# Performance work log

Measured on AMD Instinct MI355X. Metric: run time of the kernel, lower is better.

Reference implementation:

```python
import jax, jax.numpy as jnp
import numpy as np

B, N, D, F, H, C, L = 64, 8192, 5, 16, 4, 4, 4
NEG_SLOPE = 0.2


def setup_inputs() -> dict:
    key = jax.random.key(0)
    ks = jax.random.split(key, 16)
    lin = lambda k, fi, fo: (jax.random.normal(k, (fi, fo), jnp.float32) / np.sqrt(fi)).astype(jnp.float32)
    x = jax.random.normal(ks[0], (B, N, F), jnp.float32)
    agent_nodes = jax.random.randint(ks[1], (B,), 0, N, dtype=jnp.int32)
    neighbors = jax.random.randint(ks[2], (N, D), 0, N, dtype=jnp.int32)
    # GATv2 params (L layers, all 16 -> 4 heads x 4 = 16)
    Wl = jax.random.normal(ks[3], (L, F, H, C), jnp.float32) / np.sqrt(F)
    Wr = jax.random.normal(ks[4], (L, F, H, C), jnp.float32) / np.sqrt(F)
    att_w = jax.random.normal(ks[5], (L, H, C), jnp.float32) / np.sqrt(C)
    bias = jnp.zeros((L, H * C), jnp.float32)
    # global classifier 16->32->64, edge classifier 99->16->8->1
    Wg1, bg1 = lin(ks[6], H * C, 2 * H * C), jnp.zeros(2 * H * C, jnp.float32)
    Wg2, bg2 = lin(ks[7], 2 * H * C, 4 * H * C), jnp.zeros(4 * H * C, jnp.float32)
    e_in = 2 * H * C + 3 + 4 * H * C  # 99
    We1, be1 = lin(ks[8], e_in, H * C), jnp.zeros(H * C, jnp.float32)
    We2, be2 = lin(ks[9], H * C, H * C // 2), jnp.zeros(H * C // 2, jnp.float32)
    We3, be3 = lin(ks[10], H * C // 2, 1), jnp.zeros(1, jnp.float32)
    return dict(x=x, agent_nodes=agent_nodes, neighbors=neighbors, Wl=Wl, Wr=Wr,
                att_w=att_w, bias=bias, Wg1=Wg1, bg1=bg1, Wg2=Wg2, bg2=bg2,
                We1=We1, be1=be1, We2=We2, be2=be2, We3=We3, be3=be3)


def _gatv2_layer(h, src, dst, wl, wr, a, b, n_nodes):
    # h: [B,N,Fin]; wl/wr: [Fin,H,C]; a: [H,C]; b: [H*C]
    xl = jnp.einsum('bnf,fhc->bnhc', h, wl)   # source transform
    xr = jnp.einsum('bnf,fhc->bnhc', h, wr)   # target transform
    hs = xl[:, src]                            # [B,E,H,C]
    ht = xr[:, dst]
    logit = jnp.einsum('behc,hc->beh', jax.nn.leaky_relu(hs + ht, NEG_SLOPE), a)
    lt = logit.transpose(1, 0, 2)              # [E,B,H] (segment ops need E first)
    m = jax.ops.segment_max(lt, dst, num_segments=n_nodes)
    w = jnp.exp(lt - m[dst])
    s = jax.ops.segment_sum(w, dst, num_segments=n_nodes)
    alpha = w / (s[dst] + 1e-16)               # [E,B,H] softmax over in-edges of dst
    msg = alpha[..., None] * hs.transpose(1, 0, 2, 3)
    out = jax.ops.segment_sum(msg, dst, num_segments=n_nodes)  # [N,B,H,C]
    return out.transpose(1, 0, 2, 3).reshape(h.shape[0], n_nodes, -1) + b


def reference(x, agent_nodes, neighbors, Wl, Wr, att_w, bias,
              Wg1, bg1, Wg2, bg2, We1, be1, We2, be2, We3, be3):
    Bn, Nn, _ = x.shape
    Dd = neighbors.shape[1]
    loop = jnp.arange(Nn, dtype=neighbors.dtype)
    src = jnp.concatenate([jnp.repeat(loop, Dd), loop])   # add_self_loops
    dst = jnp.concatenate([neighbors.reshape(-1), loop])
    h = x
    for i in range(Wl.shape[0]):
        h = _gatv2_layer(h, src, dst, Wl[i], Wr[i], att_w[i], bias[i], Nn)
    # global mean aggregation -> 2 SlimFC(tanh)
    agg = jnp.tanh(h.mean(axis=1) @ Wg1 + bg1)
    agg = jnp.tanh(agg @ Wg2 + bg2)                        # [B,64]
    # agent out-edges: source node + its D neighbors
    nb = neighbors[agent_nodes]                            # [B,D]
    bi = jnp.arange(Bn)
    source = h[bi, agent_nodes]                            # [B,16]
    target = h[bi[:, None], nb]                            # [B,D,16]
    tok = jnp.eye(3, dtype=h.dtype)                        # 3 one-hot act tokens
    feats = jnp.concatenate([
        jnp.broadcast_to(source[:, None, None, :], (Bn, 3, Dd, source.shape[-1])),
        jnp.broadcast_to(tok[None, :, None, :], (Bn, 3, Dd, 3)),
        jnp.broadcast_to(target[:, None, :, :], (Bn, 3, Dd, target.shape[-1])),
        jnp.broadcast_to(agg[:, None, None, :], (Bn, 3, Dd, agg.shape[-1])),
    ], axis=-1)                                            # [B,3,D,99]
    e = jnp.tanh(feats @ We1 + be1)
    e = jnp.tanh(e @ We2 + be2)
    e = (e @ We3 + be3)[..., 0]                            # [B,3,D]
    # logits[b, turn*D + move] (convert_multidiscrete_action_to_discrete)
    return e.reshape(Bn, 3 * Dd)
```

## Files before the change

### kernel.cpp

```cpp
#include <hip/hip_runtime.h>
#include <hip/hip_fp16.h>
#include <cmath>

#define NNODES 8192
#define NB 64
#define ND 5
#define MAXDEG 64
#define NBLK_T0 2048
#define NBLK_LAY 8192



__global__ void __launch_bounds__(256)
k_t0fill(const float* __restrict__ x, const float* __restrict__ Wl0, const float* __restrict__ Wr0,
         __half* __restrict__ xl0, __half* __restrict__ xr0,
         const int* __restrict__ agent, const int* __restrict__ nbr,
         int* __restrict__ cnt, int* __restrict__ slot, int* __restrict__ needed) {
  if (blockIdx.x >= NBLK_T0) {
    int eb = blockIdx.x - NBLK_T0;
    if (eb < 160) {
      int i = eb*256 + threadIdx.x;
      int v = nbr[i];
      int pos = atomicAdd(&cnt[v], 1);
      slot[v*MAXDEG + 1 + pos] = i/ND;
    } else if (threadIdx.x < NB) {
      int an = agent[threadIdx.x];
      needed[an] = 1;
      #pragma unroll
      for (int d = 0; d < ND; ++d) needed[nbr[an*ND + d]] = 1;
    }
    return;
  }
  int gid = blockIdx.x*blockDim.x + threadIdx.x;
  int n = gid >> 6;
  int b = gid & 63;
  const float4* src = (const float4*)(x + (((size_t)b*NNODES + n) << 4));
  float hv[16];
  #pragma unroll
  for (int q = 0; q < 4; ++q) *(float4*)(hv+4*q) = src[q];
  float yl[16], yr[16];
  #pragma unroll
  for (int j = 0; j < 16; ++j) { yl[j] = 0.f; yr[j] = 0.f; }
  #pragma unroll
  for (int f = 0; f < 16; ++f) {
    float hf = hv[f];
    #pragma unroll
    for (int j = 0; j < 16; ++j) {
      yl[j] = fmaf(hf, Wl0[f*16+j], yl[j]);
      yr[j] = fmaf(hf, Wr0[f*16+j], yr[j]);
    }
  }
  size_t idx = ((size_t)n << 10) + (b << 4);
  __half2 lh[8], rh[8];
  #pragma unroll
  for (int j = 0; j < 8; ++j) {
    lh[j] = __floats2half2_rn(yl[2*j], yl[2*j+1]);
    rh[j] = __floats2half2_rn(yr[2*j], yr[2*j+1]);
  }
  float4* ld = (float4*)(xl0 + idx);
  ld[0] = *(float4*)&lh[0]; ld[1] = *(float4*)&lh[4];
  float4* rd = (float4*)(xr0 + idx);
  rd[0] = *(float4*)&rh[0]; rd[1] = *(float4*)&rh[4];
}


template<bool LAST>
__global__ void __launch_bounds__(256)
k_layer(const __half* __restrict__ xlin, const __half* __restrict__ xrin,
        __half* __restrict__ xlout, __half* __restrict__ xrout,
        const float* __restrict__ WlNext, const float* __restrict__ WrNext,
        const float* __restrict__ att, const float* __restrict__ bias,
        const int* __restrict__ cnt, const int* __restrict__ slot,
        const int* __restrict__ needed, __half* __restrict__ h,
        float* __restrict__ meanpart) {
  __shared__ float sW[544];
  __shared__ float msm[4][16][17];
  int tid = threadIdx.x;
  int w = tid >> 6, lane = tid & 63;

  if (!LAST) {
    sW[tid]     = WlNext[tid];
    sW[256+tid] = WrNext[tid];
  }
  if (tid < 16)      sW[512+tid]    = att[tid];
  else if (tid < 32) sW[512+tid]    = bias[tid-16];
  __syncthreads();

  int wv = (blockIdx.x << 2) + w;
  int q = wv >> 13;
  int v = wv & (NNODES-1);
  int head = lane & 3;
  size_t soff = ((size_t)q << 8) + (lane << 2);

  float4 awv = *(float4*)&sW[512 + head*4];
  float aw0 = awv.x, aw1 = awv.y, aw2 = awv.z, aw3 = awv.w;

  float xr0, xr1, xr2, xr3;
  {
    float2 rx = *(const float2*)(xrin + (((size_t)v) << 10) + soff);
    __half2* ph = (__half2*)&rx;
    float2 f0 = __half22float2(ph[0]), f1 = __half22float2(ph[1]);
    xr0 = f0.x; xr1 = f0.y; xr2 = f1.x; xr3 = f1.y;
  }

  float s = 0.f, a0 = 0.f, a1 = 0.f, a2 = 0.f, a3 = 0.f;
  int deg = cnt[v];
  int tot = deg + 1;
  const int* sl = slot + v*MAXDEG;

  auto loadrow = [&](int u) -> float2 {
    return *(const float2*)(xlin + (((size_t)u) << 10) + soff);
  };
  auto process = [&](float2 r) {
    __half2* ph = (__half2*)&r;
    float2 f0 = __half22float2(ph[0]), f1 = __half22float2(ph[1]);
    float t0 = f0.x, t1 = f0.y, t2 = f1.x, t3 = f1.y;
    float z0 = t0 + xr0; z0 = (z0 >= 0.f) ? z0 : 0.2f*z0;
    float z1 = t1 + xr1; z1 = (z1 >= 0.f) ? z1 : 0.2f*z1;
    float z2 = t2 + xr2; z2 = (z2 >= 0.f) ? z2 : 0.2f*z2;
    float z3 = t3 + xr3; z3 = (z3 >= 0.f) ? z3 : 0.2f*z3;
    float lg = fmaf(z0, aw0, fmaf(z1, aw1, fmaf(z2, aw2, z3*aw3)));
    float p = __expf(lg);
    s += p;
    a0 = fmaf(p, t0, a0); a1 = fmaf(p, t1, a1);
    a2 = fmaf(p, t2, a2); a3 = fmaf(p, t3, a3);
  };

  float2 r0, r1, r2, r3, r4, r5, r6, r7, pA, pB;
  r0 = loadrow(v);
  if (tot > 1) r1 = loadrow(sl[1]);
  if (tot > 2) r2 = loadrow(sl[2]);
  if (tot > 3) r3 = loadrow(sl[3]);
  if (tot > 4) r4 = loadrow(sl[4]);
  if (tot > 5) r5 = loadrow(sl[5]);
  if (tot > 6) r6 = loadrow(sl[6]);
  if (tot > 7) r7 = loadrow(sl[7]);
  if (tot > 8) pA = loadrow(sl[8]);
  if (tot > 9) pB = loadrow(sl[9]);
  process(r0);
  if (tot > 1) process(r1);
  if (tot > 2) process(r2);
  if (tot > 3) process(r3);
  if (tot > 4) process(r4);
  if (tot > 5) process(r5);
  if (tot > 6) process(r6);
  if (tot > 7) process(r7);
  int e = 8;
  for (; e+1 < tot; e += 2) {
    float2 cA = pA; if (e+2 < tot) pA = loadrow(sl[e+2]);
    float2 cB = pB; if (e+3 < tot) pB = loadrow(sl[e+3]);
    process(cA); process(cB);
  }
  if (e < tot) process(pA);

  float inv = 1.f / s;
  float4 bsv = *(float4*)&sW[528 + head*4];
  float o0 = fmaf(a0, inv, bsv.x), o1 = fmaf(a1, inv, bsv.y);
  float o2 = fmaf(a2, inv, bsv.z), o3 = fmaf(a3, inv, bsv.w);

  if (!LAST) {
    float of[16];
    int lb = lane & ~3;
    #pragma unroll
    for (int src = 0; src < 4; ++src) {
      of[src*4+0] = __shfl(o0, lb+src);
      of[src*4+1] = __shfl(o1, lb+src);
      of[src*4+2] = __shfl(o2, lb+src);
      of[src*4+3] = __shfl(o3, lb+src);
    }
    float yl0=0.f, yl1=0.f, yl2=0.f, yl3=0.f;
    float yr0=0.f, yr1=0.f, yr2=0.f, yr3=0.f;
    #pragma unroll
    for (int f = 0; f < 16; ++f) {
      float4 wl4 = *(float4*)&sW[f*16 + head*4];
      float4 wr4 = *(float4*)&sW[256 + f*16 + head*4];
      float ofv = of[f];
      yl0 = fmaf(ofv, wl4.x, yl0); yl1 = fmaf(ofv, wl4.y, yl1);
      yl2 = fmaf(ofv, wl4.z, yl2); yl3 = fmaf(ofv, wl4.w, yl3);
      yr0 = fmaf(ofv, wr4.x, yr0); yr1 = fmaf(ofv, wr4.y, yr1);
      yr2 = fmaf(ofv, wr4.z, yr2); yr3 = fmaf(ofv, wr4.w, yr3);
    }
    float2 lo, ro;
    ((__half2*)&lo)[0] = __floats2half2_rn(yl0, yl1);
    ((__half2*)&lo)[1] = __floats2half2_rn(yl2, yl3);
    ((__half2*)&ro)[0] = __floats2half2_rn(yr0, yr1);
    ((__half2*)&ro)[1] = __floats2half2_rn(yr2, yr3);
    size_t idx = (((size_t)v) << 10) + soff;
    *(float2*)(xlout + idx) = lo;
    *(float2*)(xrout + idx) = ro;
  } else {
    if (needed[v]) {
      float2 ho;
      ((__half2*)&ho)[0] = __floats2half2_rn(o0, o1);
      ((__half2*)&ho)[1] = __floats2half2_rn(o2, o3);
      *(float2*)(h + (((size_t)v) << 10) + soff) = ho;
    }
    int bl = lane >> 2;
    msm[w][bl][head*4+0] = o0;
    msm[w][bl][head*4+1] = o1;
    msm[w][bl][head*4+2] = o2;
    msm[w][bl][head*4+3] = o3;
    __syncthreads();
    int bl2 = tid >> 4, hc = tid & 15;
    float ssum = msm[0][bl2][hc] + msm[1][bl2][hc] + msm[2][bl2][hc] + msm[3][bl2][hc];
    meanpart[(size_t)blockIdx.x*256 + tid] = ssum;
  }
}


__global__ void __launch_bounds__(256)
k_tail(const __half* __restrict__ h, const int* __restrict__ agent,
       const int* __restrict__ nbr, const float* __restrict__ meanpart,
       const float* __restrict__ Wg1, const float* __restrict__ bg1,
       const float* __restrict__ Wg2, const float* __restrict__ bg2,
       const float* __restrict__ We1, const float* __restrict__ be1,
       const float* __restrict__ We2, const float* __restrict__ be2,
       const float* __restrict__ We3, const float* __restrict__ be3,
       float* __restrict__ out) {
  int b = blockIdx.x;
  int t = threadIdx.x;
  __shared__ float red[256];
  __shared__ float mean[16], g1[32], aggs[64];
  __shared__ float srcv[16];
  __shared__ float tgt[5][16];
  __shared__ float e1s[15][16];
  __shared__ float e2s[15][8];
  int an = agent[b];

  {
    int hc = t & 15, grp = t >> 4;
    int q = b >> 4, bl = b & 15;
    float s = 0.f;
    int base = q*2048 + grp*128;
    #pragma unroll 8
    for (int p = 0; p < 128; ++p)
      s += meanpart[(size_t)(base+p)*256 + bl*16 + hc];
    red[t] = s;
    __syncthreads();
    if (t < 16) {
      float m = 0.f;
      for (int g = 0; g < 16; ++g) m += red[g*16 + t];
      mean[t] = m * (1.0f/NNODES);
    }
  }
  if (t >= 64 && t < 80) srcv[t-64] = __half2float(h[((size_t)an << 10) + (b << 4) + (t-64)]);
  if (t >= 96 && t < 176) {
    int d = (t-96)/16, k = (t-96)%16;
    int nn = nbr[an*ND + d];
    tgt[d][k] = __half2float(h[((size_t)nn << 10) + (b << 4) + k]);
  }
  __syncthreads();
  if (t < 32) {
    float a = bg1[t];
    for (int f = 0; f < 16; ++f) a = fmaf(mean[f], Wg1[f*32+t], a);
    g1[t] = tanhf(a);
  }
  __syncthreads();
  if (t < 64) {
    float a = bg2[t];
    for (int f = 0; f < 32; ++f) a = fmaf(g1[f], Wg2[f*64+t], a);
    aggs[t] = tanhf(a);
  }
  __syncthreads();
  if (t < 240) {
    int j = t & 15, td = t >> 4;
    int tk = td/5, d = td%5;
    float a = be1[j];
    for (int k = 0; k < 16; ++k) a = fmaf(srcv[k],  We1[k*16+j],      a);
    a += We1[(16+tk)*16 + j];
    for (int k = 0; k < 16; ++k) a = fmaf(tgt[d][k], We1[(19+k)*16+j], a);
    for (int k = 0; k < 64; ++k) a = fmaf(aggs[k],  We1[(35+k)*16+j], a);
    e1s[td][j] = tanhf(a);
  }
  __syncthreads();
  if (t < 120) {
    int j = t & 7, td = t >> 3;
    float a = be2[j];
    for (int k = 0; k < 16; ++k) a = fmaf(e1s[td][k], We2[k*8+j], a);
    e2s[td][j] = tanhf(a);
  }
  __syncthreads();
  if (t < 15) {
    float a = be3[0];
    for (int k = 0; k < 8; ++k) a = fmaf(e2s[t][k], We3[k], a);
    out[b*15 + t] = a;
  }
}


extern "C" void kernel_launch(void* const* d_in, const int* in_sizes, int n_in,
                              void* d_out, int out_size, void* d_ws, size_t ws_size,
                              hipStream_t stream) {
  const float* x     = (const float*)d_in[0];
  const int*   agent = (const int*)  d_in[1];
  const int*   nbr   = (const int*)  d_in[2];
  const float* Wl    = (const float*)d_in[3];
  const float* Wr    = (const float*)d_in[4];
  const float* att   = (const float*)d_in[5];
  const float* bias  = (const float*)d_in[6];
  const float* Wg1   = (const float*)d_in[7];
  const float* bg1   = (const float*)d_in[8];
  const float* Wg2   = (const float*)d_in[9];
  const float* bg2   = (const float*)d_in[10];
  const float* We1   = (const float*)d_in[11];
  const float* be1   = (const float*)d_in[12];
  const float* We2   = (const float*)d_in[13];
  const float* be2   = (const float*)d_in[14];
  const float* We3   = (const float*)d_in[15];
  const float* be3   = (const float*)d_in[16];
  float* out = (float*)d_out;

  char* ws = (char*)d_ws;
  size_t off = 0;
  auto alloc = [&](size_t bytes) -> void* {
    void* p = ws + off;
    off += (bytes + 255) & ~(size_t)255;
    return p;
  };
  const size_t XBYTES = (size_t)NNODES*NB*16*sizeof(__half);
  __half* h    = (__half*)alloc(XBYTES);
  __half* xlA  = (__half*)alloc(XBYTES);
  __half* xlB  = (__half*)alloc(XBYTES);
  __half* xrA  = (__half*)alloc(XBYTES);
  __half* xrB  = (__half*)alloc(XBYTES);
  int*  slot   = (int*)alloc((size_t)NNODES*MAXDEG*sizeof(int));
  float* meanpart = (float*)alloc((size_t)NBLK_LAY*256*sizeof(float));
  int* cnt    = (int*)alloc(NNODES*sizeof(int));
  int* needed = (int*)alloc(NNODES*sizeof(int));

  hipMemsetAsync(cnt, 0, NNODES*sizeof(int)*2, stream);

  k_t0fill<<<NBLK_T0 + 161, 256, 0, stream>>>(x, Wl, Wr, xlA, xrA,
                                              agent, nbr, cnt, slot, needed);

  k_layer<false><<<NBLK_LAY, 256, 0, stream>>>(xlA, xrA, xlB, xrB, Wl + 256, Wr + 256,
                                               att,      bias,      cnt, slot, needed, nullptr, nullptr);
  k_layer<false><<<NBLK_LAY, 256, 0, stream>>>(xlB, xrB, xlA, xrA, Wl + 512, Wr + 512,
                                               att + 16, bias + 16, cnt, slot, needed, nullptr, nullptr);
  k_layer<false><<<NBLK_LAY, 256, 0, stream>>>(xlA, xrA, xlB, xrB, Wl + 768, Wr + 768,
                                               att + 32, bias + 32, cnt, slot, needed, nullptr, nullptr);
  k_layer<true ><<<NBLK_LAY, 256, 0, stream>>>(xlB, xrB, nullptr, nullptr, nullptr, nullptr,
                                               att + 48, bias + 48, cnt, slot, needed, h, meanpart);

  k_tail<<<NB, 256, 0, stream>>>(h, agent, nbr, meanpart,
                                 Wg1, bg1, Wg2, bg2,
                                 We1, be1, We2, be2, We3, be3, out);
}
```

Before: 244.3 us.

## Split per-node GAT work so each lane handles two channels instead of four

The layer kernel now gives each lane two feature channels (8 lanes per batch element, 8 batch elements per wavefront) instead of four channels for 16 batch elements, and doubles the number of blocks. The attention logit is completed with a cross-lane xor shuffle between the two lanes of a head. The goal is more wavefronts in flight to hide the latency of the irregular neighbor gathers, at the cost of narrower 4-byte loads, an extra shuffle per edge, and neighbor-list and index loads repeated across twice as many wavefronts. The mean-partial buffer and the tail reduction indexing are adjusted to match.

```diff
diff --git a/kernel.cpp b/kernel.cpp
--- a/kernel.cpp
+++ b/kernel.cpp
@@ -7,7 +7,7 @@
 #define ND 5
 #define MAXDEG 64
 #define NBLK_T0 2048
-#define NBLK_LAY 8192
+#define NBLK_LAY 16384
 
 
 
@@ -74,7 +74,7 @@
         const int* __restrict__ needed, __half* __restrict__ h,
         float* __restrict__ meanpart) {
   __shared__ float sW[544];
-  __shared__ float msm[4][16][17];
+  __shared__ float msm[4][8][17];
   int tid = threadIdx.x;
   int w = tid >> 6, lane = tid & 63;
 
@@ -87,46 +87,43 @@
   __syncthreads();
 
   int wv = (blockIdx.x << 2) + w;
-  int q = wv >> 13;
+  int e = wv >> 13;
   int v = wv & (NNODES-1);
-  int head = lane & 3;
-  size_t soff = ((size_t)q << 8) + (lane << 2);
-
-  float4 awv = *(float4*)&sW[512 + head*4];
-  float aw0 = awv.x, aw1 = awv.y, aw2 = awv.z, aw3 = awv.w;
-
-  float xr0, xr1, xr2, xr3;
+  int bb = lane >> 3;
+  int k  = lane & 7;
+  size_t soff = ((size_t)e << 7) + (bb << 4) + (k << 1);
+
+  float2 awv = *(float2*)&sW[512 + 2*k];
+  float aw0 = awv.x, aw1 = awv.y;
+
+  float xr0, xr1;
   {
-    float2 rx = *(const float2*)(xrin + (((size_t)v) << 10) + soff);
-    __half2* ph = (__half2*)&rx;
-    float2 f0 = __half22float2(ph[0]), f1 = __half22float2(ph[1]);
-    xr0 = f0.x; xr1 = f0.y; xr2 = f1.x; xr3 = f1.y;
-  }
-
-  float s = 0.f, a0 = 0.f, a1 = 0.f, a2 = 0.f, a3 = 0.f;
+    float rx = *(const float*)(xrin + (((size_t)v) << 10) + soff);
+    float2 f0 = __half22float2(*(__half2*)&rx);
+    xr0 = f0.x; xr1 = f0.y;
+  }
+
+  float s = 0.f, a0 = 0.f, a1 = 0.f;
   int deg = cnt[v];
   int tot = deg + 1;
   const int* sl = slot + v*MAXDEG;
 
-  auto loadrow = [&](int u) -> float2 {
-    return *(const float2*)(xlin + (((size_t)u) << 10) + soff);
+  auto loadrow = [&](int u) -> float {
+    return *(const float*)(xlin + (((size_t)u) << 10) + soff);
   };
-  auto process = [&](float2 r) {
-    __half2* ph = (__half2*)&r;
-    float2 f0 = __half22float2(ph[0]), f1 = __half22float2(ph[1]);
-    float t0 = f0.x, t1 = f0.y, t2 = f1.x, t3 = f1.y;
+  auto process = [&](float r) {
+    float2 f0 = __half22float2(*(__half2*)&r);
+    float t0 = f0.x, t1 = f0.y;
     float z0 = t0 + xr0; z0 = (z0 >= 0.f) ? z0 : 0.2f*z0;
     float z1 = t1 + xr1; z1 = (z1 >= 0.f) ? z1 : 0.2f*z1;
-    float z2 = t2 + xr2; z2 = (z2 >= 0.f) ? z2 : 0.2f*z2;
-    float z3 = t3 + xr3; z3 = (z3 >= 0.f) ? z3 : 0.2f*z3;
-    float lg = fmaf(z0, aw0, fmaf(z1, aw1, fmaf(z2, aw2, z3*aw3)));
+    float lgh = fmaf(z0, aw0, z1*aw1);
+    float lg = lgh + __shfl_xor(lgh, 1);
     float p = __expf(lg);
     s += p;
     a0 = fmaf(p, t0, a0); a1 = fmaf(p, t1, a1);
-    a2 = fmaf(p, t2, a2); a3 = fmaf(p, t3, a3);
   };
 
-  float2 r0, r1, r2, r3, r4, r5, r6, r7, pA, pB;
+  float r0, r1, r2, r3, r4, r5, r6, r7, pA, pB;
   r0 = loadrow(v);
   if (tot > 1) r1 = loadrow(sl[1]);
   if (tot > 2) r2 = loadrow(sl[2]);
@@ -145,65 +142,50 @@
   if (tot > 5) process(r5);
   if (tot > 6) process(r6);
   if (tot > 7) process(r7);
-  int e = 8;
-  for (; e+1 < tot; e += 2) {
-    float2 cA = pA; if (e+2 < tot) pA = loadrow(sl[e+2]);
-    float2 cB = pB; if (e+3 < tot) pB = loadrow(sl[e+3]);
+  int ei = 8;
+  for (; ei+1 < tot; ei += 2) {
+    float cA = pA; if (ei+2 < tot) pA = loadrow(sl[ei+2]);
+    float cB = pB; if (ei+3 < tot) pB = loadrow(sl[ei+3]);
     process(cA); process(cB);
   }
-  if (e < tot) process(pA);
+  if (ei < tot) process(pA);
 
   float inv = 1.f / s;
-  float4 bsv = *(float4*)&sW[528 + head*4];
+  float2 bsv = *(float2*)&sW[528 + 2*k];
   float o0 = fmaf(a0, inv, bsv.x), o1 = fmaf(a1, inv, bsv.y);
-  float o2 = fmaf(a2, inv, bsv.z), o3 = fmaf(a3, inv, bsv.w);
 
   if (!LAST) {
     float of[16];
-    int lb = lane & ~3;
+    int lb = lane & ~7;
     #pragma unroll
-    for (int src = 0; src < 4; ++src) {
-      of[src*4+0] = __shfl(o0, lb+src);
-      of[src*4+1] = __shfl(o1, lb+src);
-      of[src*4+2] = __shfl(o2, lb+src);
-      of[src*4+3] = __shfl(o3, lb+src);
-    }
-    float yl0=0.f, yl1=0.f, yl2=0.f, yl3=0.f;
-    float yr0=0.f, yr1=0.f, yr2=0.f, yr3=0.f;
+    for (int m = 0; m < 8; ++m) {
+      of[2*m]   = __shfl(o0, lb+m);
+      of[2*m+1] = __shfl(o1, lb+m);
+    }
+    float yl0=0.f, yl1=0.f, yr0=0.f, yr1=0.f;
     #pragma unroll
     for (int f = 0; f < 16; ++f) {
-      float4 wl4 = *(float4*)&sW[f*16 + head*4];
-      float4 wr4 = *(float4*)&sW[256 + f*16 + head*4];
+      float2 wl2 = *(float2*)&sW[f*16 + 2*k];
+      float2 wr2 = *(float2*)&sW[256 + f*16 + 2*k];
       float ofv = of[f];
-      yl0 = fmaf(ofv, wl4.x, yl0); yl1 = fmaf(ofv, wl4.y, yl1);
-      yl2 = fmaf(ofv, wl4.z, yl2); yl3 = fmaf(ofv, wl4.w, yl3);
-      yr0 = fmaf(ofv, wr4.x, yr0); yr1 = fmaf(ofv, wr4.y, yr1);
-      yr2 = fmaf(ofv, wr4.z, yr2); yr3 = fmaf(ofv, wr4.w, yr3);
-    }
-    float2 lo, ro;
-    ((__half2*)&lo)[0] = __floats2half2_rn(yl0, yl1);
-    ((__half2*)&lo)[1] = __floats2half2_rn(yl2, yl3);
-    ((__half2*)&ro)[0] = __floats2half2_rn(yr0, yr1);
-    ((__half2*)&ro)[1] = __floats2half2_rn(yr2, yr3);
+      yl0 = fmaf(ofv, wl2.x, yl0); yl1 = fmaf(ofv, wl2.y, yl1);
+      yr0 = fmaf(ofv, wr2.x, yr0); yr1 = fmaf(ofv, wr2.y, yr1);
+    }
     size_t idx = (((size_t)v) << 10) + soff;
-    *(float2*)(xlout + idx) = lo;
-    *(float2*)(xrout + idx) = ro;
+    *(__half2*)(xlout + idx) = __floats2half2_rn(yl0, yl1);
+    *(__half2*)(xrout + idx) = __floats2half2_rn(yr0, yr1);
   } else {
     if (needed[v]) {
-      float2 ho;
-      ((__half2*)&ho)[0] = __floats2half2_rn(o0, o1);
-      ((__half2*)&ho)[1] = __floats2half2_rn(o2, o3);
-      *(float2*)(h + (((size_t)v) << 10) + soff) = ho;
-    }
-    int bl = lane >> 2;
-    msm[w][bl][head*4+0] = o0;
-    msm[w][bl][head*4+1] = o1;
-    msm[w][bl][head*4+2] = o2;
-    msm[w][bl][head*4+3] = o3;
+      *(__half2*)(h + (((size_t)v) << 10) + soff) = __floats2half2_rn(o0, o1);
+    }
+    msm[w][bb][2*k]   = o0;
+    msm[w][bb][2*k+1] = o1;
     __syncthreads();
-    int bl2 = tid >> 4, hc = tid & 15;
-    float ssum = msm[0][bl2][hc] + msm[1][bl2][hc] + msm[2][bl2][hc] + msm[3][bl2][hc];
-    meanpart[(size_t)blockIdx.x*256 + tid] = ssum;
+    if (tid < 128) {
+      int bl = tid >> 4, hc = tid & 15;
+      float ssum = msm[0][bl][hc] + msm[1][bl][hc] + msm[2][bl][hc] + msm[3][bl][hc];
+      meanpart[(size_t)blockIdx.x*128 + tid] = ssum;
+    }
   }
 }
 
@@ -229,12 +211,12 @@
 
   {
     int hc = t & 15, grp = t >> 4;
-    int q = b >> 4, bl = b & 15;
+    int e = b >> 3, bl = b & 7;
     float s = 0.f;
-    int base = q*2048 + grp*128;
+    int base = e*2048 + grp*128;
     #pragma unroll 8
     for (int p = 0; p < 128; ++p)
-      s += meanpart[(size_t)(base+p)*256 + bl*16 + hc];
+      s += meanpart[(size_t)(base+p)*128 + bl*16 + hc];
     red[t] = s;
     __syncthreads();
     if (t < 16) {
@@ -324,7 +306,7 @@
   __half* xrA  = (__half*)alloc(XBYTES);
   __half* xrB  = (__half*)alloc(XBYTES);
   int*  slot   = (int*)alloc((size_t)NNODES*MAXDEG*sizeof(int));
-  float* meanpart = (float*)alloc((size_t)NBLK_LAY*256*sizeof(float));
+  float* meanpart = (float*)alloc((size_t)NBLK_LAY*128*sizeof(float));
   int* cnt    = (int*)alloc(NNODES*sizeof(int));
   int* needed = (int*)alloc(NNODES*sizeof(int));
 
```

New measurement: 309.1 us. +26.5%, slower.

## Stage input transform through LDS and fuse tail into last GAT layer

Applied to the files above, without the earlier changes.

The layer-0 transform kernel now loads 8 nodes × 64 batches of x into shared memory with coalesced float4 reads, then computes two batch outputs per thread. This replaces strided per-thread reads of x. The separate tail kernel is removed: the last layer launches 64 extra blocks that spin on a global completion counter, then run the classifier. The fusion saves one launch but depends on the extra blocks not starving the layer blocks, and it adds atomic polling overhead.

```diff
diff --git a/kernel.cpp b/kernel.cpp
--- a/kernel.cpp
+++ b/kernel.cpp
@@ -6,7 +6,7 @@
 #define NB 64
 #define ND 5
 #define MAXDEG 64
-#define NBLK_T0 2048
+#define NBLK_T0 1024
 #define NBLK_LAY 8192
 
 
@@ -31,36 +31,66 @@
     }
     return;
   }
-  int gid = blockIdx.x*blockDim.x + threadIdx.x;
-  int n = gid >> 6;
-  int b = gid & 63;
-  const float4* src = (const float4*)(x + (((size_t)b*NNODES + n) << 4));
-  float hv[16];
+  __shared__ float4 sx4[8*321 + 8];
+  int t = threadIdx.x;
+  int n0 = blockIdx.x * 8;
+
+  {
+    int ln = (t & 31) >> 2;
+    int q  = t & 3;
+    float4 v[8];
+    #pragma unroll
+    for (int it = 0; it < 8; ++it) {
+      int b = it*8 + (t >> 5);
+      v[it] = *(const float4*)(x + ((size_t)b*NNODES + n0 + ln)*16 + q*4);
+    }
+    #pragma unroll
+    for (int it = 0; it < 8; ++it) {
+      int b = it*8 + (t >> 5);
+      sx4[ln*321 + b*5 + q] = v[it];
+    }
+  }
+  __syncthreads();
+
+  int cn = t >> 5;
+  int bq = t & 31;
+  float4 outL[2][2], outR[2][2];
   #pragma unroll
-  for (int q = 0; q < 4; ++q) *(float4*)(hv+4*q) = src[q];
-  float yl[16], yr[16];
+  for (int j = 0; j < 2; ++j) {
+    int b = bq + 32*j;
+    float hv[16];
+    #pragma unroll
+    for (int q = 0; q < 4; ++q) *(float4*)(hv + 4*q) = sx4[cn*321 + b*5 + q];
+    float yl[16], yr[16];
+    #pragma unroll
+    for (int jj = 0; jj < 16; ++jj) { yl[jj] = 0.f; yr[jj] = 0.f; }
+    #pragma unroll
+    for (int f = 0; f < 16; ++f) {
+      float hf = hv[f];
+      #pragma unroll
+      for (int jj = 0; jj < 16; ++jj) {
+        yl[jj] = fmaf(hf, Wl0[f*16+jj], yl[jj]);
+        yr[jj] = fmaf(hf, Wr0[f*16+jj], yr[jj]);
+      }
+    }
+    __half2 lh[8], rh[8];
+    #pragma unroll
+    for (int jj = 0; jj < 8; ++jj) {
+      lh[jj] = __floats2half2_rn(yl[2*jj], yl[2*jj+1]);
+      rh[jj] = __floats2half2_rn(yr[2*jj], yr[2*jj+1]);
+    }
+    outL[j][0] = *(float4*)&lh[0]; outL[j][1] = *(float4*)&lh[4];
+    outR[j][0] = *(float4*)&rh[0]; outR[j][1] = *(float4*)&rh[4];
+  }
   #pragma unroll
-  for (int j = 0; j < 16; ++j) { yl[j] = 0.f; yr[j] = 0.f; }
-  #pragma unroll
-  for (int f = 0; f < 16; ++f) {
-    float hf = hv[f];
-    #pragma unroll
-    for (int j = 0; j < 16; ++j) {
-      yl[j] = fmaf(hf, Wl0[f*16+j], yl[j]);
-      yr[j] = fmaf(hf, Wr0[f*16+j], yr[j]);
-    }
-  }
-  size_t idx = ((size_t)n << 10) + (b << 4);
-  __half2 lh[8], rh[8];
-  #pragma unroll
-  for (int j = 0; j < 8; ++j) {
-    lh[j] = __floats2half2_rn(yl[2*j], yl[2*j+1]);
-    rh[j] = __floats2half2_rn(yr[2*j], yr[2*j+1]);
-  }
-  float4* ld = (float4*)(xl0 + idx);
-  ld[0] = *(float4*)&lh[0]; ld[1] = *(float4*)&lh[4];
-  float4* rd = (float4*)(xr0 + idx);
-  rd[0] = *(float4*)&rh[0]; rd[1] = *(float4*)&rh[4];
+  for (int j = 0; j < 2; ++j) {
+    int b = bq + 32*j;
+    size_t idx = (((size_t)(n0 + cn)) << 10) + (b << 4);
+    float4* ld = (float4*)(xl0 + idx);
+    ld[0] = outL[j][0]; ld[1] = outL[j][1];
+    float4* rd = (float4*)(xr0 + idx);
+    rd[0] = outR[j][0]; rd[1] = outR[j][1];
+  }
 }
 
 
@@ -72,10 +102,95 @@
         const float* __restrict__ att, const float* __restrict__ bias,
         const int* __restrict__ cnt, const int* __restrict__ slot,
         const int* __restrict__ needed, __half* __restrict__ h,
-        float* __restrict__ meanpart) {
+        float* __restrict__ meanpart,
+        const int* __restrict__ agent, const int* __restrict__ nbr,
+        const float* __restrict__ Wg1, const float* __restrict__ bg1,
+        const float* __restrict__ Wg2, const float* __restrict__ bg2,
+        const float* __restrict__ We1, const float* __restrict__ be1,
+        const float* __restrict__ We2, const float* __restrict__ be2,
+        const float* __restrict__ We3, const float* __restrict__ be3,
+        float* __restrict__ out, int* __restrict__ ctr) {
+  int tid = threadIdx.x;
+
+  if (LAST && blockIdx.x >= NBLK_LAY) {
+    int b = blockIdx.x - NBLK_LAY;
+    if (tid == 0) {
+      while (atomicAdd(ctr, 0) < NBLK_LAY) __builtin_amdgcn_s_sleep(16);
+    }
+    __syncthreads();
+    __threadfence();
+
+    __shared__ float red[256];
+    __shared__ float mean[16], g1[32], aggs[64];
+    __shared__ float srcv[16];
+    __shared__ float tgt[5][16];
+    __shared__ float e1s[15][16];
+    __shared__ float e2s[15][8];
+    int an = agent[b];
+
+    {
+      int hc = tid & 15, grp = tid >> 4;
+      int q = b >> 4, bl = b & 15;
+      float s = 0.f;
+      int base = q*2048 + grp*128;
+      #pragma unroll 8
+      for (int p = 0; p < 128; ++p)
+        s += meanpart[(size_t)(base+p)*256 + bl*16 + hc];
+      red[tid] = s;
+      __syncthreads();
+      if (tid < 16) {
+        float m = 0.f;
+        for (int g = 0; g < 16; ++g) m += red[g*16 + tid];
+        mean[tid] = m * (1.0f/NNODES);
+      }
+    }
+    if (tid >= 64 && tid < 80) srcv[tid-64] = __half2float(h[((size_t)an << 10) + (b << 4) + (tid-64)]);
+    if (tid >= 96 && tid < 176) {
+      int d = (tid-96)/16, k = (tid-96)%16;
+      int nn = nbr[an*ND + d];
+      tgt[d][k] = __half2float(h[((size_t)nn << 10) + (b << 4) + k]);
+    }
+    __syncthreads();
+    if (tid < 32) {
+      float a = bg1[tid];
+      for (int f = 0; f < 16; ++f) a = fmaf(mean[f], Wg1[f*32+tid], a);
+      g1[tid] = tanhf(a);
+    }
+    __syncthreads();
+    if (tid < 64) {
+      float a = bg2[tid];
+      for (int f = 0; f < 32; ++f) a = fmaf(g1[f], Wg2[f*64+tid], a);
+      aggs[tid] = tanhf(a);
+    }
+    __syncthreads();
+    if (tid < 240) {
+      int j = tid & 15, td = tid >> 4;
+      int tk = td/5, d = td%5;
+      float a = be1[j];
+      for (int k = 0; k < 16; ++k) a = fmaf(srcv[k],  We1[k*16+j],      a);
+      a += We1[(16+tk)*16 + j];
+      for (int k = 0; k < 16; ++k) a = fmaf(tgt[d][k], We1[(19+k)*16+j], a);
+      for (int k = 0; k < 64; ++k) a = fmaf(aggs[k],  We1[(35+k)*16+j], a);
+      e1s[td][j] = tanhf(a);
+    }
+    __syncthreads();
+    if (tid < 120) {
+      int j = tid & 7, td = tid >> 3;
+      float a = be2[j];
+      for (int k = 0; k < 16; ++k) a = fmaf(e1s[td][k], We2[k*8+j], a);
+      e2s[td][j] = tanhf(a);
+    }
+    __syncthreads();
+    if (tid < 15) {
+      float a = be3[0];
+      for (int k = 0; k < 8; ++k) a = fmaf(e2s[tid][k], We3[k], a);
+      out[b*15 + tid] = a;
+    }
+    return;
+  }
+
   __shared__ float sW[544];
   __shared__ float msm[4][16][17];
-  int tid = threadIdx.x;
   int w = tid >> 6, lane = tid & 63;
 
   if (!LAST) {
@@ -204,86 +319,8 @@
     int bl2 = tid >> 4, hc = tid & 15;
     float ssum = msm[0][bl2][hc] + msm[1][bl2][hc] + msm[2][bl2][hc] + msm[3][bl2][hc];
     meanpart[(size_t)blockIdx.x*256 + tid] = ssum;
-  }
-}
-
-
-__global__ void __launch_bounds__(256)
-k_tail(const __half* __restrict__ h, const int* __restrict__ agent,
-       const int* __restrict__ nbr, const float* __restrict__ meanpart,
-       const float* __restrict__ Wg1, const float* __restrict__ bg1,
-       const float* __restrict__ Wg2, const float* __restrict__ bg2,
-       const float* __restrict__ We1, const float* __restrict__ be1,
-       const float* __restrict__ We2, const float* __restrict__ be2,
-       const float* __restrict__ We3, const float* __restrict__ be3,
-       float* __restrict__ out) {
-  int b = blockIdx.x;
-  int t = threadIdx.x;
-  __shared__ float red[256];
-  __shared__ float mean[16], g1[32], aggs[64];
-  __shared__ float srcv[16];
-  __shared__ float tgt[5][16];
-  __shared__ float e1s[15][16];
-  __shared__ float e2s[15][8];
-  int an = agent[b];
-
-  {
-    int hc = t & 15, grp = t >> 4;
-    int q = b >> 4, bl = b & 15;
-    float s = 0.f;
-    int base = q*2048 + grp*128;
-    #pragma unroll 8
-    for (int p = 0; p < 128; ++p)
-      s += meanpart[(size_t)(base+p)*256 + bl*16 + hc];
-    red[t] = s;
-    __syncthreads();
-    if (t < 16) {
-      float m = 0.f;
-      for (int g = 0; g < 16; ++g) m += red[g*16 + t];
-      mean[t] = m * (1.0f/NNODES);
-    }
-  }
-  if (t >= 64 && t < 80) srcv[t-64] = __half2float(h[((size_t)an << 10) + (b << 4) + (t-64)]);
-  if (t >= 96 && t < 176) {
-    int d = (t-96)/16, k = (t-96)%16;
-    int nn = nbr[an*ND + d];
-    tgt[d][k] = __half2float(h[((size_t)nn << 10) + (b << 4) + k]);
-  }
-  __syncthreads();
-  if (t < 32) {
-    float a = bg1[t];
-    for (int f = 0; f < 16; ++f) a = fmaf(mean[f], Wg1[f*32+t], a);
-    g1[t] = tanhf(a);
-  }
-  __syncthreads();
-  if (t < 64) {
-    float a = bg2[t];
-    for (int f = 0; f < 32; ++f) a = fmaf(g1[f], Wg2[f*64+t], a);
-    aggs[t] = tanhf(a);
-  }
-  __syncthreads();
-  if (t < 240) {
-    int j = t & 15, td = t >> 4;
-    int tk = td/5, d = td%5;
-    float a = be1[j];
-    for (int k = 0; k < 16; ++k) a = fmaf(srcv[k],  We1[k*16+j],      a);
-    a += We1[(16+tk)*16 + j];
-    for (int k = 0; k < 16; ++k) a = fmaf(tgt[d][k], We1[(19+k)*16+j], a);
-    for (int k = 0; k < 64; ++k) a = fmaf(aggs[k],  We1[(35+k)*16+j], a);
-    e1s[td][j] = tanhf(a);
-  }
-  __syncthreads();
-  if (t < 120) {
-    int j = t & 7, td = t >> 3;
-    float a = be2[j];
-    for (int k = 0; k < 16; ++k) a = fmaf(e1s[td][k], We2[k*8+j], a);
-    e2s[td][j] = tanhf(a);
-  }
-  __syncthreads();
-  if (t < 15) {
-    float a = be3[0];
-    for (int k = 0; k < 8; ++k) a = fmaf(e2s[t][k], We3[k], a);
-    out[b*15 + t] = a;
+    __syncthreads();
+    if (tid == 0) { __threadfence(); atomicAdd(ctr, 1); }
   }
 }
 
@@ -327,22 +364,31 @@
   float* meanpart = (float*)alloc((size_t)NBLK_LAY*256*sizeof(float));
   int* cnt    = (int*)alloc(NNODES*sizeof(int));
   int* needed = (int*)alloc(NNODES*sizeof(int));
-
-  hipMemsetAsync(cnt, 0, NNODES*sizeof(int)*2, stream);
+  int* ctr    = (int*)alloc(256);
+
+  hipMemsetAsync(cnt, 0, NNODES*sizeof(int)*2 + 256, stream);
 
   k_t0fill<<<NBLK_T0 + 161, 256, 0, stream>>>(x, Wl, Wr, xlA, xrA,
                                               agent, nbr, cnt, slot, needed);
 
   k_layer<false><<<NBLK_LAY, 256, 0, stream>>>(xlA, xrA, xlB, xrB, Wl + 256, Wr + 256,
-                                               att,      bias,      cnt, slot, needed, nullptr, nullptr);
+                                               att,      bias,      cnt, slot, needed, nullptr, nullptr,
+                                               nullptr, nullptr, nullptr, nullptr, nullptr, nullptr,
+                                               nullptr, nullptr, nullptr, nullptr, nullptr, nullptr,
+                                               nullptr, nullptr);
   k_layer<false><<<NBLK_LAY, 256, 0, stream>>>(xlB, xrB, xlA, xrA, Wl + 512, Wr + 512,
-                                               att + 16, bias + 16, cnt, slot, needed, nullptr, nullptr);
+                                               att + 16, bias + 16, cnt, slot, needed, nullptr, nullptr,
+                                               nullptr, nullptr, nullptr, nullptr, nullptr, nullptr,
+                                               nullptr, nullptr, nullptr, nullptr, nullptr, nullptr,
+                                               nullptr, nullptr);
   k_layer<false><<<NBLK_LAY, 256, 0, stream>>>(xlA, xrA, xlB, xrB, Wl + 768, Wr + 768,
-                                               att + 32, bias + 32, cnt, slot, needed, nullptr, nullptr);
-  k_layer<true ><<<NBLK_LAY, 256, 0, stream>>>(xlB, xrB, nullptr, nullptr, nullptr, nullptr,
-                                               att + 48, bias + 48, cnt, slot, needed, h, meanpart);
-
-  k_tail<<<NB, 256, 0, stream>>>(h, agent, nbr, meanpart,
-                                 Wg1, bg1, Wg2, bg2,
-                                 We1, be1, We2, be2, We3, be3, out);
+                                               att + 32, bias + 32, cnt, slot, needed, nullptr, nullptr,
+                                               nullptr, nullptr, nullptr, nullptr, nullptr, nullptr,
+                                               nullptr, nullptr, nullptr, nullptr, nullptr, nullptr,
+                                               nullptr, nullptr);
+  k_layer<true ><<<NBLK_LAY + NB, 256, 0, stream>>>(xlB, xrB, nullptr, nullptr, nullptr, nullptr,
+                                               att + 48, bias + 48, cnt, slot, needed, h, meanpart,
+                                               agent, nbr, Wg1, bg1, Wg2, bg2,
+                                               We1, be1, We2, be2, We3, be3,
+                                               out, ctr);
 }
```

After: 493.8 us. 102% more time.

## Stage layer-0 input through shared memory for coalesced loads and two batches per thread

Applied to the files above, without the earlier changes.

Each block of the layer-0 transform kernel now handles 8 nodes across all 64 batches. It loads x with coalesced float4 reads, where neighbouring lanes cover consecutive nodes and quarters, and transposes the data through padded shared memory. Each thread then computes two batch rows. Before this, each thread read 64 bytes at a stride of N*16 floats across batches, which left global reads poorly coalesced. The cost is about 41 KB of shared memory per block, which may cap occupancy, and the block count is halved.

```diff
diff --git a/kernel.cpp b/kernel.cpp
--- a/kernel.cpp
+++ b/kernel.cpp
@@ -6,7 +6,7 @@
 #define NB 64
 #define ND 5
 #define MAXDEG 64
-#define NBLK_T0 2048
+#define NBLK_T0 1024
 #define NBLK_LAY 8192
 
 
@@ -31,36 +31,66 @@
     }
     return;
   }
-  int gid = blockIdx.x*blockDim.x + threadIdx.x;
-  int n = gid >> 6;
-  int b = gid & 63;
-  const float4* src = (const float4*)(x + (((size_t)b*NNODES + n) << 4));
-  float hv[16];
+  __shared__ float4 sx4[8*321 + 8];
+  int t = threadIdx.x;
+  int n0 = blockIdx.x * 8;
+
+  {
+    int ln = (t & 31) >> 2;
+    int q  = t & 3;
+    float4 v[8];
+    #pragma unroll
+    for (int it = 0; it < 8; ++it) {
+      int b = it*8 + (t >> 5);
+      v[it] = *(const float4*)(x + ((size_t)b*NNODES + n0 + ln)*16 + q*4);
+    }
+    #pragma unroll
+    for (int it = 0; it < 8; ++it) {
+      int b = it*8 + (t >> 5);
+      sx4[ln*321 + b*5 + q] = v[it];
+    }
+  }
+  __syncthreads();
+
+  int cn = t >> 5;
+  int bq = t & 31;
+  float4 outL[2][2], outR[2][2];
   #pragma unroll
-  for (int q = 0; q < 4; ++q) *(float4*)(hv+4*q) = src[q];
-  float yl[16], yr[16];
+  for (int j = 0; j < 2; ++j) {
+    int b = bq + 32*j;
+    float hv[16];
+    #pragma unroll
+    for (int q = 0; q < 4; ++q) *(float4*)(hv + 4*q) = sx4[cn*321 + b*5 + q];
+    float yl[16], yr[16];
+    #pragma unroll
+    for (int jj = 0; jj < 16; ++jj) { yl[jj] = 0.f; yr[jj] = 0.f; }
+    #pragma unroll
+    for (int f = 0; f < 16; ++f) {
+      float hf = hv[f];
+      #pragma unroll
+      for (int jj = 0; jj < 16; ++jj) {
+        yl[jj] = fmaf(hf, Wl0[f*16+jj], yl[jj]);
+        yr[jj] = fmaf(hf, Wr0[f*16+jj], yr[jj]);
+      }
+    }
+    __half2 lh[8], rh[8];
+    #pragma unroll
+    for (int jj = 0; jj < 8; ++jj) {
+      lh[jj] = __floats2half2_rn(yl[2*jj], yl[2*jj+1]);
+      rh[jj] = __floats2half2_rn(yr[2*jj], yr[2*jj+1]);
+    }
+    outL[j][0] = *(float4*)&lh[0]; outL[j][1] = *(float4*)&lh[4];
+    outR[j][0] = *(float4*)&rh[0]; outR[j][1] = *(float4*)&rh[4];
+  }
   #pragma unroll
-  for (int j = 0; j < 16; ++j) { yl[j] = 0.f; yr[j] = 0.f; }
-  #pragma unroll
-  for (int f = 0; f < 16; ++f) {
-    float hf = hv[f];
-    #pragma unroll
-    for (int j = 0; j < 16; ++j) {
-      yl[j] = fmaf(hf, Wl0[f*16+j], yl[j]);
-      yr[j] = fmaf(hf, Wr0[f*16+j], yr[j]);
-    }
-  }
-  size_t idx = ((size_t)n << 10) + (b << 4);
-  __half2 lh[8], rh[8];
-  #pragma unroll
-  for (int j = 0; j < 8; ++j) {
-    lh[j] = __floats2half2_rn(yl[2*j], yl[2*j+1]);
-    rh[j] = __floats2half2_rn(yr[2*j], yr[2*j+1]);
-  }
-  float4* ld = (float4*)(xl0 + idx);
-  ld[0] = *(float4*)&lh[0]; ld[1] = *(float4*)&lh[4];
-  float4* rd = (float4*)(xr0 + idx);
-  rd[0] = *(float4*)&rh[0]; rd[1] = *(float4*)&rh[4];
+  for (int j = 0; j < 2; ++j) {
+    int b = bq + 32*j;
+    size_t idx = (((size_t)(n0 + cn)) << 10) + (b << 4);
+    float4* ld = (float4*)(xl0 + idx);
+    ld[0] = outL[j][0]; ld[1] = outL[j][1];
+    float4* rd = (float4*)(xr0 + idx);
+    rd[0] = outR[j][0]; rd[1] = outR[j][1];
+  }
 }
 
 
```

Measured after the change: 246.9 us. About the same (+1.1%).
